# Kernel tuning notes

Measured on AMD Instinct MI355X. Metric: run time of the kernel, lower is better.

## Reference

```python
import jax, jax.numpy as jnp
import numpy as np

B, N, E, R = 2, 4096, 1024, 128   # batch, seq_len, embed_dim, expand_ratio (head_dim)
H = E // R                        # num heads (scalar decay per head)
EPS = 1e-5                        # torch LayerNorm default eps


def _silu(x):
    return x * jax.nn.sigmoid(x)


def setup_inputs() -> dict:
    key = jax.random.key(0)
    ks = jax.random.split(key, 12)
    std = 0.02

    def w(k, shape):
        return jax.random.normal(k, shape, jnp.float32) * std

    return {
        "x": jax.random.normal(ks[0], (B, N, E), jnp.float32),
        # log of lower bound of the decay gate; must be negative so exp() in (0,1)
        "log_lower_bound": -jax.random.uniform(ks[1], (H,), jnp.float32, minval=0.1, maxval=3.0),
        "Wq": w(ks[2], (E, E)),
        "Wk": w(ks[3], (E, E)),
        "Wv": w(ks[4], (E, E)),
        "Wf": w(ks[5], (H, E)),      # f_proj: embed_dim -> embed_dim // expand_ratio
        "Wb1": w(ks[6], (R, E)),     # bet_proj low-rank
        "Wb2": w(ks[7], (E, R)),
        "Wg1": w(ks[8], (R, E)),     # output_gate low-rank
        "Wg2": w(ks[9], (E, R)),
        "gamma": jnp.ones((E,), jnp.float32),  # LayerNorm weight (bias=False)
        "Wo": w(ks[10], (E, E)),
    }


def _simple_gla(q, k, v, g):
    """Gated linear attention recurrence (fla simple_gla semantics).
    q,k,v: [B,H,N,R]; g: [B,H,N] (log decay per head per step).
    S_t = exp(g_t) * S_{t-1} + k_t v_t^T ;  o_t = (q_t * d^-0.5) @ S_t
    """
    scale = q.shape[-1] ** -0.5
    qT = jnp.moveaxis(q, 2, 0)  # [N,B,H,R]
    kT = jnp.moveaxis(k, 2, 0)
    vT = jnp.moveaxis(v, 2, 0)
    gT = jnp.moveaxis(g, 2, 0)  # [N,B,H]

    S0 = jnp.zeros((q.shape[0], q.shape[1], q.shape[-1], v.shape[-1]), q.dtype)

    def step(S, inp):
        qt, kt, vt, gt = inp
        S = S * jnp.exp(gt)[..., None, None] + kt[..., :, None] * vt[..., None, :]
        o = jnp.einsum('bhk,bhkv->bhv', qt * scale, S)
        return S, o

    _, o = jax.lax.scan(step, S0, (qT, kT, vT, gT))
    return jnp.moveaxis(o, 0, 2)  # [B,H,N,R]


def reference(x, log_lower_bound, Wq, Wk, Wv, Wf, Wb1, Wb2, Wg1, Wg2, gamma, Wo):
    # projections + activations
    q = _silu(x @ Wq.T)
    k = _silu(x @ Wk.T)
    v = x @ Wv.T
    f = x @ Wf.T                      # [B,N,H] scalar decay logits per head

    # householder q-transform with dense-memory beta (normalized reflection vector)
    beta = _silu((x @ Wb1.T) @ Wb2.T)  # [B,N,E]
    bn = beta * jax.lax.rsqrt(jnp.sum(beta * beta, -1, keepdims=True) + 1e-12)
    q = q - 2.0 * jnp.sum(q * bn, -1, keepdims=True) * bn

    def split_heads(t):  # [B,N,E] -> [B,H,N,R]
        return jnp.moveaxis(t.reshape(B, N, H, R), 2, 1)

    qh, kh, vh = split_heads(q), split_heads(k), split_heads(v)

    # log-space decay gate with lower bound
    lb = jnp.exp(log_lower_bound)                      # [H] in (0,1)
    fg = lb + (1.0 - lb) * jax.nn.sigmoid(f)           # [B,N,H]
    log_f = jnp.transpose(jnp.log(fg), (0, 2, 1))      # [B,H,N]

    o = _simple_gla(qh, kh, vh, log_f)                 # [B,H,N,R]
    o = jnp.moveaxis(o, 1, 2).reshape(B, N, E)

    # output gate
    gate = jax.nn.sigmoid((x @ Wg1.T) @ Wg2.T)
    o = o * gate

    # LayerNorm (weight only, bias=False)
    mu = jnp.mean(o, -1, keepdims=True)
    var = jnp.mean((o - mu) ** 2, -1, keepdims=True)
    o = (o - mu) * jax.lax.rsqrt(var + EPS) * gamma

    return o @ Wo.T
```

## Files before the change

### kernel.cpp

```cpp
#include <hip/hip_runtime.h>
#include <hip/hip_bf16.h>

using u16 = unsigned short;
typedef __attribute__((ext_vector_type(8))) short bf16x8;
typedef __attribute__((ext_vector_type(4))) float f32x4;
typedef __attribute__((ext_vector_type(8))) u16 u16x8;
typedef __attribute__((ext_vector_type(4))) u16 u16x4;

#define B_ 2
#define N_ 4096
#define E_ 1024
#define R_ 128
#define H_ 8
#define M_ 8192
#define CHUNK_ 128
#define NC_ 32
#define BH_ 16

__device__ __forceinline__ float b2f(u16 u) { return __uint_as_float(((unsigned)u) << 16); }
__device__ __forceinline__ u16 f2b(float f) {
  unsigned u = __float_as_uint(f);
  return (u16)((u + 0x7fffu + ((u >> 16) & 1u)) >> 16);
}
__device__ __forceinline__ float sigm(float x) {
  return __builtin_amdgcn_rcpf(1.0f + __expf(-x));
}

#define GLDS(g, l) __builtin_amdgcn_global_load_lds( \
    (const __attribute__((address_space(1))) unsigned int*)(g), \
    (__attribute__((address_space(3))) unsigned int*)(l), 16, 0, 0)

struct CvtArgs {
  const float* src[10];
  u16* dst[11];
};

__global__ void __launch_bounds__(256) cvt_all(CvtArgs a) {
  int idx = blockIdx.x * 256 + threadIdx.x;
  const int SZ[11] = {2097152, 262144, 262144, 262144, 2048,
                      32768, 32768, 32768, 32768, 262144, 30720};
  int off = idx, seg = 0;
#pragma unroll
  for (int i = 0; i < 10; i++) {
    if (seg == i && off >= SZ[i]) { off -= SZ[i]; seg = i + 1; }
  }
  u16x4 z = (u16x4){0, 0, 0, 0};
  if (seg == 10) { ((u16x4*)a.dst[10])[off] = z; return; }
  float4 v = ((const float4*)a.src[seg])[off];
  u16x4 r;
  r[0] = f2b(v.x); r[1] = f2b(v.y); r[2] = f2b(v.z); r[3] = f2b(v.w);
  if (seg == 6) {
    int n = off >> 5, c = off & 31;
    u16x4* W2 = (u16x4*)a.dst[6];
    W2[n * 64 + c] = r; W2[n * 64 + 32 + c] = z;
  } else if (seg == 8) {
    int n = off >> 5, c = off & 31;
    u16x4* W2 = (u16x4*)a.dst[8];
    W2[(1024 + n) * 64 + 32 + c] = r; W2[(1024 + n) * 64 + c] = z;
  } else {
    ((u16x4*)a.dst[seg])[off] = r;
  }
}

template<bool SWAP>
__device__ __forceinline__ void mfma_panel(f32x4 (&acc)[4][4], const u16* A, const u16* Bm,
                                           int wr, int wc, int l15, int q8) {
  bf16x8 af[4], bf[4];
#pragma unroll
  for (int mi = 0; mi < 4; mi++) af[mi] = *(const bf16x8*)&A[(wr * 64 + mi * 16 + l15) * 32 + q8];
#pragma unroll
  for (int ni = 0; ni < 4; ni++) bf[ni] = *(const bf16x8*)&Bm[(wc * 64 + ni * 16 + l15) * 32 + q8];
#pragma unroll
  for (int mi = 0; mi < 4; mi++)
#pragma unroll
    for (int ni = 0; ni < 4; ni++)
      acc[mi][ni] = SWAP
        ? __builtin_amdgcn_mfma_f32_16x16x32_bf16(bf[ni], af[mi], acc[mi][ni], 0, 0, 0)
        : __builtin_amdgcn_mfma_f32_16x16x32_bf16(af[mi], bf[ni], acc[mi][ni], 0, 0, 0);
}

template<bool SWAP>
__device__ __forceinline__ void gemm_loop(const u16* __restrict__ X, const u16* __restrict__ W,
                                          int m0, int n0, int K,
                                          u16* As, u16* Bs, f32x4 (&acc)[4][4], int tid) {
  const int wave = tid >> 6, lane = tid & 63;
  const int wr = wave >> 1, wc = wave & 1, l15 = lane & 15, q8 = (lane >> 4) * 8;
  const u16* Ap = X + (size_t)(m0 + wave * 32 + (lane >> 2)) * K + (lane & 3) * 8;
  const u16* Bp = W + (size_t)(n0 + wave * 32 + (lane >> 2)) * K + (lane & 3) * 8;
  u16* A0 = As + wave * 1024;
  u16* B0 = Bs + wave * 1024;
  for (int k0 = 0; k0 < K; k0 += 64) {
    GLDS(Ap + k0,                    A0);
    GLDS(Ap + 16 * (size_t)K + k0,   A0 + 512);
    GLDS(Ap + k0 + 32,               A0 + 4096);
    GLDS(Ap + 16 * (size_t)K + k0 + 32, A0 + 4608);
    GLDS(Bp + k0,                    B0);
    GLDS(Bp + 16 * (size_t)K + k0,   B0 + 512);
    GLDS(Bp + k0 + 32,               B0 + 4096);
    GLDS(Bp + 16 * (size_t)K + k0 + 32, B0 + 4608);
    __syncthreads();
    mfma_panel<SWAP>(acc, As, Bs, wr, wc, l15, q8);
    mfma_panel<SWAP>(acc, As + 4096, Bs + 4096, wr, wc, l15, q8);
    __syncthreads();
  }
}

__global__ void __launch_bounds__(256) mega_gemm(const u16* __restrict__ X, const u16* __restrict__ Wcat,
                                                 const float* __restrict__ llb,
                                                 u16* __restrict__ Qb, u16* __restrict__ Kb,
                                                 u16* __restrict__ KT, u16* __restrict__ VT,
                                                 u16* __restrict__ T1, float* __restrict__ LOGF) {
  __shared__ u16 sh[17408];
  u16* As = sh;
  u16* Bs = sh + 8192;
  u16* Ts = sh;
  const int tid = threadIdx.x;
  const int m0 = blockIdx.x * 128;
  const int ny = blockIdx.y, n0 = ny * 128;
  const int wave = tid >> 6, lane = tid & 63;
  const int wr = wave >> 1, wc = wave & 1, l15 = lane & 15, q4 = (lane >> 4) * 4;
  f32x4 acc[4][4];
#pragma unroll
  for (int i = 0; i < 4; i++)
#pragma unroll
    for (int j = 0; j < 4; j++) acc[i][j] = (f32x4){0.f, 0.f, 0.f, 0.f};

  if (ny >= 16 && ny < 24) {
    gemm_loop<false>(X, Wcat, m0, n0, 1024, As, Bs, acc, tid);
#pragma unroll
    for (int mi = 0; mi < 4; mi++) {
#pragma unroll
      for (int ni = 0; ni < 4; ni++) {
        int col = n0 - 2048 + wc * 64 + ni * 16 + l15;
        int rbase = m0 + wr * 64 + mi * 16 + q4;
        int head = col >> 7, rl = col & 127;
        int bb = rbase >> 12, nseq = rbase & (N_ - 1);
        u16x4 pk;
#pragma unroll
        for (int r = 0; r < 4; r++) pk[r] = f2b(acc[mi][ni][r]);
        *(u16x4*)&VT[((size_t)(bb * H_ + head) * R_ + rl) * N_ + nseq] = pk;
      }
    }
    return;
  }

  gemm_loop<true>(X, Wcat, m0, n0, 1024, As, Bs, acc, tid);

  if (ny == 26) {
    if (wc == 0 && (lane >> 4) < 2) {
#pragma unroll
      for (int mi = 0; mi < 4; mi++) {
        int mcol = m0 + wr * 64 + mi * 16 + l15;
        int bb = mcol >> 12, nseq = mcol & (N_ - 1);
#pragma unroll
        for (int r = 0; r < 4; r++) {
          int h = q4 + r;
          float lb = __expf(llb[h]);
          LOGF[(size_t)(bb * H_ + h) * N_ + nseq] =
              __logf(lb + (1.f - lb) * sigm(acc[mi][0][r]));
        }
      }
    }
    return;
  }

#pragma unroll
  for (int mi = 0; mi < 4; mi++) {
#pragma unroll
    for (int ni = 0; ni < 4; ni++) {
      int nb = n0 + wc * 64 + ni * 16 + q4;
      int mcol = m0 + wr * 64 + mi * 16 + l15;
      u16x4 pk;
#pragma unroll
      for (int r = 0; r < 4; r++) {
        float v = acc[mi][ni][r];
        if (ny < 16) v = v * sigm(v);
        pk[r] = f2b(v);
      }
      if (ny < 8) {
        *(u16x4*)&Qb[(size_t)mcol * E_ + nb] = pk;
      } else if (ny < 16) {
        *(u16x4*)&Kb[(size_t)mcol * E_ + nb - 1024] = pk;
        int nl = nb - n0;
        int ml = mcol - m0;
#pragma unroll
        for (int r = 0; r < 4; r++) Ts[(nl + r) * 136 + ml] = pk[r];
      } else {
        *(u16x4*)&T1[(size_t)mcol * 256 + nb - 3072] = pk;
      }
    }
  }

  if (ny >= 8 && ny < 16) {
    __syncthreads();
    int head = (n0 - 1024) >> 7;
    int bb = m0 >> 12, nloc = m0 & (N_ - 1);
    size_t base = ((size_t)(bb * H_ + head) * R_) * N_ + nloc;
#pragma unroll
    for (int p = 0; p < 8; p++) {
      int nl = p * 16 + (tid >> 4);
      int m8 = (tid & 15) * 8;
      u16x8 v = *(const u16x8*)&Ts[nl * 136 + m8];
      *(u16x8*)&KT[base + (size_t)nl * N_ + m8] = v;
    }
  }
}

__global__ void __launch_bounds__(256) bg_gemm(const u16* __restrict__ T1, const u16* __restrict__ W2,
                                               u16* __restrict__ BETA, u16* __restrict__ GATE) {
  __shared__ u16 As[8192];
  __shared__ u16 Bs[8192];
  const int tid = threadIdx.x;
  const int m0 = blockIdx.x * 128;
  const int n0 = blockIdx.y * 128;
  f32x4 acc[4][4];
#pragma unroll
  for (int i = 0; i < 4; i++)
#pragma unroll
    for (int j = 0; j < 4; j++) acc[i][j] = (f32x4){0.f, 0.f, 0.f, 0.f};
  gemm_loop<true>(T1, W2, m0, n0, 256, As, Bs, acc, tid);
  const int wave = tid >> 6, lane = tid & 63;
  const int wr = wave >> 1, wc = wave & 1, l15 = lane & 15, q4 = (lane >> 4) * 4;
#pragma unroll
  for (int mi = 0; mi < 4; mi++) {
#pragma unroll
    for (int ni = 0; ni < 4; ni++) {
      int nb = n0 + wc * 64 + ni * 16 + q4;
      int mcol = m0 + wr * 64 + mi * 16 + l15;
      u16x4 pk;
      if (nb < 1024) {
#pragma unroll
        for (int r = 0; r < 4; r++) {
          float v = acc[mi][ni][r];
          pk[r] = f2b(v * sigm(v));
        }
        *(u16x4*)&BETA[(size_t)mcol * E_ + nb] = pk;
      } else {
#pragma unroll
        for (int r = 0; r < 4; r++) pk[r] = f2b(sigm(acc[mi][ni][r]));
        *(u16x4*)&GATE[(size_t)mcol * E_ + nb - 1024] = pk;
      }
    }
  }
}

__global__ void __launch_bounds__(256) out_gemm(const u16* __restrict__ X, const u16* __restrict__ W,
                                                float* __restrict__ C) {
  __shared__ u16 As[8192];
  __shared__ u16 Bs[8192];
  const int tid = threadIdx.x;
  const int m0 = blockIdx.x * 128;
  const int n0 = blockIdx.y * 128;
  f32x4 acc[4][4];
#pragma unroll
  for (int i = 0; i < 4; i++)
#pragma unroll
    for (int j = 0; j < 4; j++) acc[i][j] = (f32x4){0.f, 0.f, 0.f, 0.f};
  gemm_loop<true>(X, W, m0, n0, 1024, As, Bs, acc, tid);
  const int wave = tid >> 6, lane = tid & 63;
  const int wr = wave >> 1, wc = wave & 1, l15 = lane & 15, q4 = (lane >> 4) * 4;
#pragma unroll
  for (int mi = 0; mi < 4; mi++) {
#pragma unroll
    for (int ni = 0; ni < 4; ni++) {
      int nb = n0 + wc * 64 + ni * 16 + q4;
      int mcol = m0 + wr * 64 + mi * 16 + l15;
      *(f32x4*)&C[(size_t)mcol * E_ + nb] = acc[mi][ni];
    }
  }
}

__global__ void __launch_bounds__(256) householder(u16* __restrict__ Q, const u16* __restrict__ BETA) {
  int row = blockIdx.x;
  int tid = threadIdx.x;
  u16* q = Q + (size_t)row * E_;
  const u16* bt = BETA + (size_t)row * E_;
  u16x4 q4 = *(const u16x4*)(q + tid * 4);
  u16x4 b4 = *(const u16x4*)(bt + tid * 4);
  float qv[4], bv[4];
#pragma unroll
  for (int i = 0; i < 4; i++) { qv[i] = b2f(q4[i]); bv[i] = b2f(b4[i]); }
  float ss = bv[0]*bv[0] + bv[1]*bv[1] + bv[2]*bv[2] + bv[3]*bv[3];
  float qd = qv[0]*bv[0] + qv[1]*bv[1] + qv[2]*bv[2] + qv[3]*bv[3];
  __shared__ float red[8];
#pragma unroll
  for (int m = 1; m < 64; m <<= 1) { ss += __shfl_xor(ss, m); qd += __shfl_xor(qd, m); }
  int wid = tid >> 6;
  if ((tid & 63) == 0) { red[wid] = ss; red[4 + wid] = qd; }
  __syncthreads();
  ss = red[0] + red[1] + red[2] + red[3];
  qd = red[4] + red[5] + red[6] + red[7];
  float coef = 2.f * qd / (ss + 1e-12f);
  const float scale = 0.08838834764831845f;
  u16x4 o4;
#pragma unroll
  for (int i = 0; i < 4; i++) o4[i] = f2b((qv[i] - coef * bv[i]) * scale);
  *(u16x4*)(q + tid * 4) = o4;
}

__device__ __forceinline__ void scan_chunk(const float* __restrict__ lf, float* cum, int tid) {
  if (tid < 64) {
    float a = lf[tid], b = lf[tid + 64];
#pragma unroll
    for (int off = 1; off < 64; off <<= 1) {
      float t = __shfl_up(a, off);  if (tid >= off) a += t;
      float t2 = __shfl_up(b, off); if (tid >= off) b += t2;
    }
    b += __shfl(a, 63);
    cum[tid] = a; cum[tid + 64] = b;
  }
  __syncthreads();
}

__device__ __forceinline__ void stage32(u16* dst, const u16* src, size_t stride, int tid) {
  int r0 = tid >> 2, c8 = (tid & 3) * 8;
  *(u16x8*)&dst[(size_t)r0 * 40 + c8] = *(const u16x8*)&src[(size_t)r0 * stride + c8];
  int r1 = r0 + 64;
  *(u16x8*)&dst[(size_t)r1 * 40 + c8] = *(const u16x8*)&src[(size_t)r1 * stride + c8];
}

__device__ __forceinline__ void stage32_scaled(u16* dst, const u16* src, size_t stride,
                                               const float* w, int j0, int tid) {
  int c8 = (tid & 3) * 8;
  float wv[8];
#pragma unroll
  for (int i = 0; i < 8; i++) wv[i] = w[j0 + c8 + i];
#pragma unroll
  for (int rr = 0; rr < 128; rr += 64) {
    int r = rr + (tid >> 2);
    u16x8 raw = *(const u16x8*)&src[(size_t)r * stride + c8];
    u16x8 o;
#pragma unroll
    for (int i = 0; i < 8; i++) o[i] = f2b(b2f(raw[i]) * wv[i]);
    *(u16x8*)&dst[(size_t)r * 40 + c8] = o;
  }
}

template<bool SWAP>
__device__ __forceinline__ void mfma16(f32x4 (&acc)[4][4], const u16* A, const u16* Bm,
                                       int wr, int wc, int l15, int q8) {
  bf16x8 af[4], bf[4];
#pragma unroll
  for (int mi = 0; mi < 4; mi++) af[mi] = *(const bf16x8*)&A[(wr * 64 + mi * 16 + l15) * 40 + q8];
#pragma unroll
  for (int ni = 0; ni < 4; ni++) bf[ni] = *(const bf16x8*)&Bm[(wc * 64 + ni * 16 + l15) * 40 + q8];
#pragma unroll
  for (int mi = 0; mi < 4; mi++)
#pragma unroll
    for (int ni = 0; ni < 4; ni++)
      acc[mi][ni] = SWAP
        ? __builtin_amdgcn_mfma_f32_16x16x32_bf16(bf[ni], af[mi], acc[mi][ni], 0, 0, 0)
        : __builtin_amdgcn_mfma_f32_16x16x32_bf16(af[mi], bf[ni], acc[mi][ni], 0, 0, 0);
}

__global__ void __launch_bounds__(256) gla_phaseA(const u16* __restrict__ KT, const u16* __restrict__ VT,
                                                  const float* __restrict__ LOGF,
                                                  float* __restrict__ U, float* __restrict__ DC) {
  const int blk = blockIdx.x;
  const int bh = blk >> 5, c = blk & 31;
  const int tid = threadIdx.x;
  const int wave = tid >> 6, lane = tid & 63;
  const int wr = wave >> 1, wc = wave & 1, l15 = lane & 15, q8 = (lane >> 4) * 8;
  __shared__ u16 SA[128 * 40];
  __shared__ u16 SB[128 * 40];
  __shared__ float cum[CHUNK_];
  __shared__ float wd[CHUNK_];
  scan_chunk(LOGF + (size_t)bh * N_ + c * CHUNK_, cum, tid);
  if (tid < 128) wd[tid] = __expf(cum[127] - cum[tid]);
  __syncthreads();
  const u16* vbase = VT + ((size_t)bh * R_) * N_ + (size_t)c * CHUNK_;
  const u16* kbase = KT + ((size_t)bh * R_) * N_ + (size_t)c * CHUNK_;
  f32x4 acc[4][4];
#pragma unroll
  for (int i = 0; i < 4; i++)
#pragma unroll
    for (int j = 0; j < 4; j++) acc[i][j] = (f32x4){0.f, 0.f, 0.f, 0.f};
  for (int j0 = 0; j0 < CHUNK_; j0 += 32) {
    __syncthreads();
    stage32(SA, vbase + j0, N_, tid);
    stage32_scaled(SB, kbase + j0, N_, wd, j0, tid);
    __syncthreads();
    mfma16<true>(acc, SA, SB, wr, wc, l15, q8);
  }
  float* Up = U + (size_t)blk * (R_ * R_);
  const int q4 = (lane >> 4) * 4;
#pragma unroll
  for (int mi = 0; mi < 4; mi++) {
#pragma unroll
    for (int ni = 0; ni < 4; ni++) {
      int v = wr * 64 + mi * 16 + l15;
      int kb = wc * 64 + ni * 16 + q4;
      *(f32x4*)&Up[(size_t)v * R_ + kb] = acc[mi][ni];
    }
  }
  if (tid == 0) DC[blk] = __expf(cum[127]);
}

__global__ void __launch_bounds__(256) gla_phaseB(const float* __restrict__ U, const float* __restrict__ DC,
                                                  u16* __restrict__ SSb) {
  int idx = blockIdx.x * 256 + threadIdx.x;
  int bh = idx >> 14;
  int e = idx & 16383;
  float s = 0.f;
  for (int c = 0; c < NC_; c++) {
    size_t off = ((size_t)bh * NC_ + c) * 16384 + e;
    SSb[off] = f2b(s);
    s = DC[bh * NC_ + c] * s + U[off];
  }
}

__global__ void __launch_bounds__(256) gla_phaseC(const u16* __restrict__ Qb, const u16* __restrict__ Kb,
                                                  const u16* __restrict__ VT, const u16* __restrict__ SSb,
                                                  const float* __restrict__ LOGF, u16* __restrict__ Ob) {
  const int blk = blockIdx.x;
  const int bh = blk >> 5, c = blk & 31;
  const int b = bh >> 3, h = bh & 7;
  const int tid = threadIdx.x;
  const int wave = tid >> 6, lane = tid & 63;
  const int wr = wave >> 1, wc = wave & 1, l15 = lane & 15;
  const int q4i = (lane >> 4) * 4, q8 = (lane >> 4) * 8;
  __shared__ u16 SA[128 * 40];
  __shared__ u16 SB[128 * 40];
  __shared__ u16 Ps[128 * 136];
  __shared__ float cum[CHUNK_];
  __shared__ float cumE[CHUNK_];
  scan_chunk(LOGF + (size_t)bh * N_ + c * CHUNK_, cum, tid);
  if (tid < 128) cumE[tid] = __expf(cum[tid]);
  __syncthreads();
  const size_t rowbase = ((size_t)(b * N_ + c * CHUNK_)) * E_ + (size_t)h * R_;
  const u16* vtbase = VT + ((size_t)bh * R_) * N_ + (size_t)c * CHUNK_;
  const u16* ssbase = SSb + (size_t)blk * (R_ * R_);

  f32x4 acc[4][4];
#pragma unroll
  for (int i = 0; i < 4; i++)
#pragma unroll
    for (int j = 0; j < 4; j++) acc[i][j] = (f32x4){0.f, 0.f, 0.f, 0.f};

  for (int r0 = 0; r0 < R_; r0 += 32) {
    __syncthreads();
    stage32(SA, Kb + rowbase + r0, E_, tid);
    stage32(SB, Qb + rowbase + r0, E_, tid);
    __syncthreads();
    mfma16<false>(acc, SA, SB, wr, wc, l15, q8);
  }
#pragma unroll
  for (int mi = 0; mi < 4; mi++) {
#pragma unroll
    for (int ni = 0; ni < 4; ni++) {
      int jb = wr * 64 + mi * 16 + q4i;
      int i = wc * 64 + ni * 16 + l15;
      float ci = cum[i];
      float4 cj = *(const float4*)&cum[jb];
      u16x4 pk;
      float cjv[4] = {cj.x, cj.y, cj.z, cj.w};
#pragma unroll
      for (int r = 0; r < 4; r++) {
        int j = jb + r;
        float w = (j <= i) ? __expf(ci - cjv[r]) : 0.f;
        pk[r] = f2b(acc[mi][ni][r] * w);
      }
      *(u16x4*)&Ps[i * 136 + jb] = pk;
    }
  }
#pragma unroll
  for (int i = 0; i < 4; i++)
#pragma unroll
    for (int j = 0; j < 4; j++) acc[i][j] = (f32x4){0.f, 0.f, 0.f, 0.f};
  for (int k0 = 0; k0 < R_; k0 += 32) {
    __syncthreads();
    stage32(SA, Qb + rowbase + k0, E_, tid);
    stage32(SB, ssbase + k0, R_, tid);
    __syncthreads();
    mfma16<true>(acc, SA, SB, wr, wc, l15, q8);
  }
#pragma unroll
  for (int mi = 0; mi < 4; mi++) {
    float ei = cumE[wr * 64 + mi * 16 + l15];
#pragma unroll
    for (int ni = 0; ni < 4; ni++)
#pragma unroll
      for (int r = 0; r < 4; r++) acc[mi][ni][r] *= ei;
  }
  for (int j0 = 0; j0 < CHUNK_; j0 += 32) {
    __syncthreads();
    stage32(SB, vtbase + j0, N_, tid);
    __syncthreads();
    if (wr == 1 || j0 < 64) {
      bf16x8 af[4], bf[4];
#pragma unroll
      for (int mi = 0; mi < 4; mi++)
        af[mi] = *(const bf16x8*)&Ps[(wr * 64 + mi * 16 + l15) * 136 + j0 + q8];
#pragma unroll
      for (int ni = 0; ni < 4; ni++)
        bf[ni] = *(const bf16x8*)&SB[(wc * 64 + ni * 16 + l15) * 40 + q8];
#pragma unroll
      for (int mi = 0; mi < 4; mi++)
#pragma unroll
        for (int ni = 0; ni < 4; ni++)
          acc[mi][ni] = __builtin_amdgcn_mfma_f32_16x16x32_bf16(bf[ni], af[mi], acc[mi][ni], 0, 0, 0);
    }
  }
#pragma unroll
  for (int mi = 0; mi < 4; mi++) {
#pragma unroll
    for (int ni = 0; ni < 4; ni++) {
      int i = wr * 64 + mi * 16 + l15;
      int vb = wc * 64 + ni * 16 + q4i;
      u16x4 pk;
#pragma unroll
      for (int r = 0; r < 4; r++) pk[r] = f2b(acc[mi][ni][r]);
      *(u16x4*)&Ob[rowbase + (size_t)i * E_ + vb] = pk;
    }
  }
}

__global__ void __launch_bounds__(256) gate_ln(const u16* __restrict__ O, const u16* __restrict__ G,
                                               const float* __restrict__ gamma, u16* __restrict__ OLN) {
  int row = blockIdx.x, tid = threadIdx.x;
  u16x4 o4 = *(const u16x4*)(O + (size_t)row * E_ + tid * 4);
  u16x4 g4 = *(const u16x4*)(G + (size_t)row * E_ + tid * 4);
  float x0 = b2f(o4[0]) * b2f(g4[0]), x1 = b2f(o4[1]) * b2f(g4[1]);
  float x2 = b2f(o4[2]) * b2f(g4[2]), x3 = b2f(o4[3]) * b2f(g4[3]);
  float s = x0 + x1 + x2 + x3;
  float sq = x0 * x0 + x1 * x1 + x2 * x2 + x3 * x3;
  __shared__ float red[8];
#pragma unroll
  for (int m = 1; m < 64; m <<= 1) { s += __shfl_xor(s, m); sq += __shfl_xor(sq, m); }
  int wid = tid >> 6;
  if ((tid & 63) == 0) { red[wid] = s; red[4 + wid] = sq; }
  __syncthreads();
  s = red[0] + red[1] + red[2] + red[3];
  sq = red[4] + red[5] + red[6] + red[7];
  float mu = s * (1.f / 1024.f);
  float var = sq * (1.f / 1024.f) - mu * mu;
  float rs = rsqrtf(var + 1e-5f);
  int e = tid * 4;
  u16x4 r4;
  r4[0] = f2b((x0 - mu) * rs * gamma[e + 0]);
  r4[1] = f2b((x1 - mu) * rs * gamma[e + 1]);
  r4[2] = f2b((x2 - mu) * rs * gamma[e + 2]);
  r4[3] = f2b((x3 - mu) * rs * gamma[e + 3]);
  *(u16x4*)(OLN + (size_t)row * E_ + e) = r4;
}

extern "C" void kernel_launch(void* const* d_in, const int* in_sizes, int n_in,
                              void* d_out, int out_size, void* d_ws, size_t ws_size,
                              hipStream_t stream) {
  (void)in_sizes; (void)n_in; (void)out_size; (void)ws_size;
  const float* x   = (const float*)d_in[0];
  const float* llb = (const float*)d_in[1];
  const float* Wq  = (const float*)d_in[2];
  const float* Wk  = (const float*)d_in[3];
  const float* Wv  = (const float*)d_in[4];
  const float* Wf  = (const float*)d_in[5];
  const float* Wb1 = (const float*)d_in[6];
  const float* Wb2 = (const float*)d_in[7];
  const float* Wg1 = (const float*)d_in[8];
  const float* Wg2 = (const float*)d_in[9];
  const float* gm  = (const float*)d_in[10];
  const float* Wo  = (const float*)d_in[11];
  float* out = (float*)d_out;

  char* ws = (char*)d_ws;
  const size_t SZB = (size_t)M_ * E_ * 2;
  u16*   Qb    = (u16*)(ws + 0 * SZB);
  u16*   Kb    = (u16*)(ws + 1 * SZB);
  u16*   KT    = (u16*)(ws + 2 * SZB);
  u16*   VT    = (u16*)(ws + 3 * SZB);
  u16*   BETAb = (u16*)(ws + 4 * SZB);
  u16*   GATEb = (u16*)(ws + 5 * SZB);
  u16*   SSb   = (u16*)(ws + 6 * SZB);
  u16*   XB    = (u16*)(ws + 7 * SZB);
  float* U     = (float*)(ws + 8 * SZB);
  char*  tail  = ws + 8 * SZB + (size_t)BH_ * NC_ * R_ * R_ * 4;
  u16*   Wcat  = (u16*)tail;
  u16*   Wcat2 = Wcat + (size_t)3456 * 1024;
  u16*   WOb   = Wcat2 + (size_t)2048 * 256;
  u16*   T1    = WOb + (size_t)E_ * E_;
  float* LOGF  = (float*)(T1 + (size_t)M_ * 256);
  float* DC    = LOGF + (size_t)BH_ * N_;
  u16*   Ob    = BETAb;
  u16*   OLN   = Qb;

  CvtArgs ca;
  ca.src[0] = x;   ca.dst[0]  = XB;
  ca.src[1] = Wq;  ca.dst[1]  = Wcat;
  ca.src[2] = Wk;  ca.dst[2]  = Wcat + (size_t)1024 * 1024;
  ca.src[3] = Wv;  ca.dst[3]  = Wcat + (size_t)2048 * 1024;
  ca.src[4] = Wf;  ca.dst[4]  = Wcat + (size_t)3328 * 1024;
  ca.src[5] = Wb1; ca.dst[5]  = Wcat + (size_t)3072 * 1024;
  ca.src[6] = Wb2; ca.dst[6]  = Wcat2;
  ca.src[7] = Wg1; ca.dst[7]  = Wcat + (size_t)3200 * 1024;
  ca.src[8] = Wg2; ca.dst[8]  = Wcat2;
  ca.src[9] = Wo;  ca.dst[9]  = WOb;
  ca.dst[10] = Wcat + (size_t)3336 * 1024;

  dim3 blk(256);
  cvt_all<<<dim3(12928), blk, 0, stream>>>(ca);
  mega_gemm<<<dim3(64, 27), blk, 0, stream>>>(XB, Wcat, llb, Qb, Kb, KT, VT, T1, LOGF);
  bg_gemm<<<dim3(64, 16), blk, 0, stream>>>(T1, Wcat2, BETAb, GATEb);
  householder<<<dim3(M_), blk, 0, stream>>>(Qb, BETAb);
  gla_phaseA<<<dim3(BH_ * NC_), blk, 0, stream>>>(KT, VT, LOGF, U, DC);
  gla_phaseB<<<dim3(BH_ * 16384 / 256), blk, 0, stream>>>(U, DC, SSb);
  gla_phaseC<<<dim3(BH_ * NC_), blk, 0, stream>>>(Qb, Kb, VT, SSb, LOGF, Ob);
  gate_ln<<<dim3(M_), blk, 0, stream>>>(Ob, GATEb, gm, OLN);
  out_gemm<<<dim3(64, 8), blk, 0, stream>>>(OLN, WOb, out);
}
```

Measured before the change: 316.6 us.

## Store chunk state in bf16, swap mega_gemm grid order, unroll GEMM K loop

Three unrelated changes. The per-chunk state U written by gla_phaseA and read by gla_phaseB becomes bf16 instead of fp32, halving that buffer's traffic at some cost in precision in the inter-chunk scan. The mega_gemm grid is transposed so consecutive blocks share the same row tile of X across output columns, which changes L2 reuse. The GEMM K dimension becomes a template parameter so the K loop can be fully unrolled, which may raise code size.

```diff
diff --git a/kernel.cpp b/kernel.cpp
--- a/kernel.cpp
+++ b/kernel.cpp
@@ -79,9 +79,9 @@
         : __builtin_amdgcn_mfma_f32_16x16x32_bf16(af[mi], bf[ni], acc[mi][ni], 0, 0, 0);
 }
 
-template<bool SWAP>
+template<bool SWAP, int K>
 __device__ __forceinline__ void gemm_loop(const u16* __restrict__ X, const u16* __restrict__ W,
-                                          int m0, int n0, int K,
+                                          int m0, int n0,
                                           u16* As, u16* Bs, f32x4 (&acc)[4][4], int tid) {
   const int wave = tid >> 6, lane = tid & 63;
   const int wr = wave >> 1, wc = wave & 1, l15 = lane & 15, q8 = (lane >> 4) * 8;
@@ -89,6 +89,7 @@
   const u16* Bp = W + (size_t)(n0 + wave * 32 + (lane >> 2)) * K + (lane & 3) * 8;
   u16* A0 = As + wave * 1024;
   u16* B0 = Bs + wave * 1024;
+#pragma unroll
   for (int k0 = 0; k0 < K; k0 += 64) {
     GLDS(Ap + k0,                    A0);
     GLDS(Ap + 16 * (size_t)K + k0,   A0 + 512);
@@ -115,8 +116,8 @@
   u16* Bs = sh + 8192;
   u16* Ts = sh;
   const int tid = threadIdx.x;
-  const int m0 = blockIdx.x * 128;
-  const int ny = blockIdx.y, n0 = ny * 128;
+  const int m0 = blockIdx.y * 128;
+  const int ny = blockIdx.x, n0 = ny * 128;
   const int wave = tid >> 6, lane = tid & 63;
   const int wr = wave >> 1, wc = wave & 1, l15 = lane & 15, q4 = (lane >> 4) * 4;
   f32x4 acc[4][4];
@@ -126,7 +127,7 @@
     for (int j = 0; j < 4; j++) acc[i][j] = (f32x4){0.f, 0.f, 0.f, 0.f};
 
   if (ny >= 16 && ny < 24) {
-    gemm_loop<false>(X, Wcat, m0, n0, 1024, As, Bs, acc, tid);
+    gemm_loop<false, 1024>(X, Wcat, m0, n0, As, Bs, acc, tid);
 #pragma unroll
     for (int mi = 0; mi < 4; mi++) {
 #pragma unroll
@@ -144,7 +145,7 @@
     return;
   }
 
-  gemm_loop<true>(X, Wcat, m0, n0, 1024, As, Bs, acc, tid);
+  gemm_loop<true, 1024>(X, Wcat, m0, n0, As, Bs, acc, tid);
 
   if (ny == 26) {
     if (wc == 0 && (lane >> 4) < 2) {
@@ -218,7 +219,7 @@
   for (int i = 0; i < 4; i++)
 #pragma unroll
     for (int j = 0; j < 4; j++) acc[i][j] = (f32x4){0.f, 0.f, 0.f, 0.f};
-  gemm_loop<true>(T1, W2, m0, n0, 256, As, Bs, acc, tid);
+  gemm_loop<true, 256>(T1, W2, m0, n0, As, Bs, acc, tid);
   const int wave = tid >> 6, lane = tid & 63;
   const int wr = wave >> 1, wc = wave & 1, l15 = lane & 15, q4 = (lane >> 4) * 4;
 #pragma unroll
@@ -256,7 +257,7 @@
   for (int i = 0; i < 4; i++)
 #pragma unroll
     for (int j = 0; j < 4; j++) acc[i][j] = (f32x4){0.f, 0.f, 0.f, 0.f};
-  gemm_loop<true>(X, W, m0, n0, 1024, As, Bs, acc, tid);
+  gemm_loop<true, 1024>(X, W, m0, n0, As, Bs, acc, tid);
   const int wave = tid >> 6, lane = tid & 63;
   const int wr = wave >> 1, wc = wave & 1, l15 = lane & 15, q4 = (lane >> 4) * 4;
 #pragma unroll
@@ -355,7 +356,7 @@
 
 __global__ void __launch_bounds__(256) gla_phaseA(const u16* __restrict__ KT, const u16* __restrict__ VT,
                                                   const float* __restrict__ LOGF,
-                                                  float* __restrict__ U, float* __restrict__ DC) {
+                                                  u16* __restrict__ U, float* __restrict__ DC) {
   const int blk = blockIdx.x;
   const int bh = blk >> 5, c = blk & 31;
   const int tid = threadIdx.x;
@@ -382,7 +383,7 @@
     __syncthreads();
     mfma16<true>(acc, SA, SB, wr, wc, l15, q8);
   }
-  float* Up = U + (size_t)blk * (R_ * R_);
+  u16* Up = U + (size_t)blk * (R_ * R_);
   const int q4 = (lane >> 4) * 4;
 #pragma unroll
   for (int mi = 0; mi < 4; mi++) {
@@ -390,13 +391,16 @@
     for (int ni = 0; ni < 4; ni++) {
       int v = wr * 64 + mi * 16 + l15;
       int kb = wc * 64 + ni * 16 + q4;
-      *(f32x4*)&Up[(size_t)v * R_ + kb] = acc[mi][ni];
+      u16x4 pk;
+#pragma unroll
+      for (int r = 0; r < 4; r++) pk[r] = f2b(acc[mi][ni][r]);
+      *(u16x4*)&Up[(size_t)v * R_ + kb] = pk;
     }
   }
   if (tid == 0) DC[blk] = __expf(cum[127]);
 }
 
-__global__ void __launch_bounds__(256) gla_phaseB(const float* __restrict__ U, const float* __restrict__ DC,
+__global__ void __launch_bounds__(256) gla_phaseB(const u16* __restrict__ U, const float* __restrict__ DC,
                                                   u16* __restrict__ SSb) {
   int idx = blockIdx.x * 256 + threadIdx.x;
   int bh = idx >> 14;
@@ -405,7 +409,7 @@
   for (int c = 0; c < NC_; c++) {
     size_t off = ((size_t)bh * NC_ + c) * 16384 + e;
     SSb[off] = f2b(s);
-    s = DC[bh * NC_ + c] * s + U[off];
+    s = DC[bh * NC_ + c] * s + b2f(U[off]);
   }
 }
 
@@ -572,8 +576,8 @@
   u16*   GATEb = (u16*)(ws + 5 * SZB);
   u16*   SSb   = (u16*)(ws + 6 * SZB);
   u16*   XB    = (u16*)(ws + 7 * SZB);
-  float* U     = (float*)(ws + 8 * SZB);
-  char*  tail  = ws + 8 * SZB + (size_t)BH_ * NC_ * R_ * R_ * 4;
+  u16*   U     = (u16*)(ws + 8 * SZB);
+  char*  tail  = ws + 8 * SZB + (size_t)BH_ * NC_ * R_ * R_ * 2;
   u16*   Wcat  = (u16*)tail;
   u16*   Wcat2 = Wcat + (size_t)3456 * 1024;
   u16*   WOb   = Wcat2 + (size_t)2048 * 256;
@@ -598,7 +602,7 @@
 
   dim3 blk(256);
   cvt_all<<<dim3(12928), blk, 0, stream>>>(ca);
-  mega_gemm<<<dim3(64, 27), blk, 0, stream>>>(XB, Wcat, llb, Qb, Kb, KT, VT, T1, LOGF);
+  mega_gemm<<<dim3(27, 64), blk, 0, stream>>>(XB, Wcat, llb, Qb, Kb, KT, VT, T1, LOGF);
   bg_gemm<<<dim3(64, 16), blk, 0, stream>>>(T1, Wcat2, BETAb, GATEb);
   householder<<<dim3(M_), blk, 0, stream>>>(Qb, BETAb);
   gla_phaseA<<<dim3(BH_ * NC_), blk, 0, stream>>>(KT, VT, LOGF, U, DC);
```

Measured after the change: 308.3 us. 2.6% less time.
